# Kernel tuning notes

Hardware: AMD Instinct MI355X
Metric: run time of the kernel (lower is better)

Reference implementation:

```python
import jax, jax.numpy as jnp
from jax import lax
import numpy as np

# Config matching init_kwargs
NUM_CLASSES = 19
K = 200               # keep_k_centers
NMS_KERNEL = 9
CENTER_THR = 0.1
LABEL_DIV = 256
VOID = 255
STUFF_AREA = 4096
THING_IDS = np.array([11, 12, 13, 14, 15, 16, 17, 18])
IS_THING = jnp.zeros(NUM_CLASSES, bool).at[jnp.asarray(THING_IDS)].set(True)


def _process_one(logits, heat, offset):
    # logits [C,H,W], heat [1,H,W], offset [2,H,W]
    C, H, W = logits.shape
    sem = jnp.argmax(logits, axis=0).astype(jnp.int32)          # [H,W]
    h = heat[0]
    ht = jnp.where(h > CENTER_THR, h, 0.0)
    pad = NMS_KERNEL // 2
    # torch max_pool2d pads implicitly with -inf
    pooled = lax.reduce_window(ht, -jnp.inf, lax.max,
                               (NMS_KERNEL, NMS_KERNEL), (1, 1),
                               ((pad, pad), (pad, pad)))
    nms = jnp.where(ht == pooled, ht, 0.0)                      # [H,W]
    flat = nms.reshape(-1)
    scores, idx = lax.top_k(flat, K)                            # fixed-size center set
    valid = scores > 0.0
    num_pos = jnp.sum(flat > 0.0)
    # Match torch ordering: if more than K peaks -> topk (descending-score) order;
    # otherwise nonzero() row-major order. Invalid slots pushed to the end.
    big = jnp.int32(H * W + K)
    order_key = jnp.where(valid,
                          jnp.where(num_pos > K,
                                    jnp.arange(K, dtype=jnp.int32),
                                    idx.astype(jnp.int32)),
                          big)
    perm = jnp.argsort(order_key)
    idx = idx[perm]
    valid = valid[perm]
    FAR = 1e9  # invalid centers placed infinitely far away
    cy = jnp.where(valid, (idx // W).astype(jnp.float32), FAR)
    cx = jnp.where(valid, (idx % W).astype(jnp.float32), FAR)
    ty = jnp.arange(H, dtype=jnp.float32)[:, None] + offset[0]  # [H,W]
    tx = jnp.arange(W, dtype=jnp.float32)[None, :] + offset[1]  # [H,W]
    # squared distances [H,W,K]; argmin equals argmin of cdist
    d2 = (ty[..., None] - cy) ** 2 + (tx[..., None] - cx) ** 2
    closest = jnp.argmin(d2, axis=-1).astype(jnp.int32)         # [H,W]
    thing_mask = IS_THING[sem]
    inst = jnp.where(thing_mask & valid.any(), closest + 1, 0).astype(jnp.int32)
    # Majority class per instance via (instance, class) histogram.
    # argmax picks the smallest class among ties, matching torch.mode.
    hist = jnp.zeros((K + 1) * NUM_CLASSES, jnp.int32)
    hist = hist.at[(inst * NUM_CLASSES + sem).reshape(-1)].add(1)
    hist = hist.reshape(K + 1, NUM_CLASSES)
    majority = jnp.argmax(hist, axis=1).astype(jnp.int32)       # [K+1]
    pan = jnp.where(inst > 0, majority[inst] * LABEL_DIV + inst, VOID * LABEL_DIV)
    # Stuff: per-class pixel counts restricted to non-instance pixels
    stuff_pix = inst == 0
    skey = jnp.where(stuff_pix, sem, NUM_CLASSES).reshape(-1)
    scounts = jnp.zeros(NUM_CLASSES + 1, jnp.int32).at[skey].add(1)[:NUM_CLASSES]
    cond = stuff_pix & (~thing_mask) & (scounts[sem] >= STUFF_AREA)
    pan = jnp.where(cond, sem * LABEL_DIV, pan)
    return pan.astype(jnp.int32), inst


def setup_inputs() -> dict:
    key = jax.random.key(0)
    k1, k2, k3 = jax.random.split(key, 3)
    B, C, H, W = 2, NUM_CLASSES, 512, 1024
    semantic_logits = jax.random.normal(k1, (B, C, H, W), dtype=jnp.float32)
    center_heatmap = jax.random.uniform(k2, (B, 1, H, W), dtype=jnp.float32)
    offset_map = jax.random.normal(k3, (B, 2, H, W), dtype=jnp.float32)
    return {"semantic_logits": semantic_logits,
            "center_heatmap": center_heatmap,
            "offset_map": offset_map}


def reference(semantic_logits, center_heatmap, offset_map):
    pan, inst = jax.vmap(_process_one)(semantic_logits, center_heatmap, offset_map)
    return pan, inst
```

## Files before the change

### kernel.cpp

```cpp
#include <hip/hip_runtime.h>

#define B 2
#define C 19
#define H 512
#define W 1024
#define HW (H*W)
#define K 200
#define CAP 16384
#define SL 7680
#define NCLS 19
#define HISTN ((K+1)*NCLS)

typedef unsigned long long u64;


__global__ void k_zero(int* __restrict__ ws) {
    int i = blockIdx.x * 256 + threadIdx.x;
    if (i < 7680) ws[i] = 0;
}

__global__ __launch_bounds__(256) void k_nms(const float* __restrict__ heat,
                                             u64* __restrict__ keys,
                                             int* __restrict__ cnt) {
    __shared__ float ht[40][40];
    __shared__ float hm[40][32];
    __shared__ u64 lpk[1024];
    __shared__ int lcnt, gbase;
    int b = blockIdx.z;
    int x0 = blockIdx.x * 32, y0 = blockIdx.y * 32;
    int tid = threadIdx.y * 32 + threadIdx.x;
    const float* hb = heat + (size_t)b * HW;
    if (tid == 0) lcnt = 0;
    for (int i = tid; i < 40 * 40; i += 256) {
        int ly = i / 40, lx = i % 40;
        int gy = y0 + ly - 4, gx = x0 + lx - 4;
        float v = 0.f;
        if (gy >= 0 && gy < H && gx >= 0 && gx < W) {
            float hv = hb[gy * W + gx];
            v = (hv > 0.1f) ? hv : 0.f;
        }
        ht[ly][lx] = v;
    }
    __syncthreads();
    for (int i = tid; i < 40 * 32; i += 256) {
        int ly = i >> 5, lx = i & 31;
        float m = ht[ly][lx];
#pragma unroll
        for (int d = 1; d < 9; ++d) m = fmaxf(m, ht[ly][lx + d]);
        hm[ly][lx] = m;
    }
    __syncthreads();
#pragma unroll
    for (int r = 0; r < 4; ++r) {
        int oy = threadIdx.y + r * 8;
        int ox = threadIdx.x;
        float c = ht[oy + 4][ox + 4];
        if (c > 0.f) {
            float m = hm[oy][ox];
#pragma unroll
            for (int d = 1; d < 9; ++d) m = fmaxf(m, hm[oy + d][ox]);
            if (c == m) {
                int pos = atomicAdd(&lcnt, 1);
                unsigned sb = __float_as_uint(c);
                lpk[pos] = ((u64)(~sb) << 19)
                         | (unsigned)((y0 + oy) * W + (x0 + ox));
            }
        }
    }
    __syncthreads();
    if (tid == 0 && lcnt > 0) gbase = atomicAdd(&cnt[b], lcnt);
    __syncthreads();
    for (int i = tid; i < lcnt; i += 256) {
        int gp = gbase + i;
        if (gp < CAP) keys[(size_t)b * CAP + gp] = lpk[i];
    }
}

__global__ __launch_bounds__(1024) void k_topk(const u64* __restrict__ keys,
                                               const int* __restrict__ cnt,
                                               int* __restrict__ anyv,
                                               float* __restrict__ cy,
                                               float* __restrict__ cx) {
    __shared__ u64 skeys[SL];
    __shared__ int hcnt[256];
    __shared__ u64 cand[256];
    __shared__ u64 s_thr;
    __shared__ int sR, gcnt;
    int b = blockIdx.x, tid = threadIdx.x;
    int lane = tid & 63;
    const u64* kb = keys + (size_t)b * CAP;
    int N = cnt[b];
    int M = (N < CAP) ? N : CAP;
    int Ksel = (M < K) ? M : K;
    for (int i = tid; i < M && i < SL; i += 1024) skeys[i] = kb[i];
    if (tid == 0) { s_thr = 0ULL; sR = Ksel; gcnt = 0; }
    __syncthreads();
    u64 thr;
    if (M <= K) {
        thr = ~0ULL;
    } else {
#pragma unroll 1
        for (int d = 48; d >= 0; d -= 8) {
            if (tid < 256) hcnt[tid] = 0;
            __syncthreads();
            u64 pref = s_thr;
            for (int i = tid; i < M; i += 1024) {
                u64 kk = (i < SL) ? skeys[i] : kb[i];
                int dig = (int)((kk >> d) & 255ULL);
                if (d == 48) {
                    u64 mask = __ballot(1);
                    while (mask) {
                        int leader = __ffsll(mask) - 1;
                        int d0 = __shfl(dig, leader, 64);
                        u64 same = __ballot(dig == d0);
                        if (lane == leader) atomicAdd(&hcnt[d0], (int)__popcll(same));
                        mask &= ~same;
                    }
                } else {
                    if ((kk >> (d + 8)) == (pref >> (d + 8)))
                        atomicAdd(&hcnt[dig], 1);
                }
            }
            __syncthreads();
            if (tid < 64) {
                int h0 = hcnt[tid * 4 + 0], h1 = hcnt[tid * 4 + 1];
                int h2 = hcnt[tid * 4 + 2], h3 = hcnt[tid * 4 + 3];
                int s = h0 + h1 + h2 + h3;
                int incl = s;
#pragma unroll
                for (int off = 1; off < 64; off <<= 1) {
                    int v = __shfl_up(incl, off, 64);
                    if (tid >= off) incl += v;
                }
                int R = sR;
                int before = incl - s;
                if (before < R && R <= incl) {
                    int c = before, t = tid * 4;
                    if (c + h0 < R) { c += h0; t++;
                        if (c + h1 < R) { c += h1; t++;
                            if (c + h2 < R) { c += h2; t++; } } }
                    s_thr = pref | ((u64)t << d);
                    sR = R - c;
                }
            }
            __syncthreads();
        }
        thr = s_thr;
    }
    for (int i = tid; i < M; i += 1024) {
        u64 kk = (i < SL) ? skeys[i] : kb[i];
        if (kk <= thr) {
            int p = atomicAdd(&gcnt, 1);
            if (p < 256) cand[p] = kk;
        }
    }
    __syncthreads();
    if (tid < 256) {
        int g = (gcnt < 256) ? gcnt : 256;
        u64 v = (tid < g) ? cand[tid] : ~0ULL;
        if (N <= K && tid < g) v &= 0x7FFFFULL;
        cand[tid] = v;
    }
    __syncthreads();
    if (tid < 256) {
        u64 v = cand[tid];
        int r = 0;
        for (int j = 0; j < 256; ++j) {
            u64 cj = cand[j];
            r += (int)((cj < v) || (cj == v && j < tid));
        }
        skeys[r] = v;
    }
    __syncthreads();
    if (tid < K) {
        bool valid = tid < Ksel;
        unsigned idx = (unsigned)(skeys[tid] & 0x7FFFFULL);
        cy[b * K + tid] = valid ? (float)(idx >> 10) : 1e9f;
        cx[b * K + tid] = valid ? (float)(idx & 1023) : 1e9f;
    }
    if (tid == 0) anyv[b] = (N > 0) ? 1 : 0;
}

__global__ __launch_bounds__(256) void k_inst(const float* __restrict__ logits,
                                              const float* __restrict__ offs,
                                              const float* __restrict__ gcy,
                                              const float* __restrict__ gcx,
                                              const int* __restrict__ anyv,
                                              int* __restrict__ semout,
                                              int* __restrict__ inst,
                                              int* __restrict__ hist) {
    __shared__ int lh[HISTN];
    __shared__ float scy[K], scx[K];
    __shared__ unsigned char skk[K];
    __shared__ float red[4][8];
    __shared__ int wcnt[4];
    int b = blockIdx.z;
    int x0 = blockIdx.x << 5, y0 = blockIdx.y << 5;
    int tid = threadIdx.x;
    int lane = tid & 63, w = tid >> 6;
    for (int i = tid; i < HISTN; i += 256) lh[i] = 0;
    int r = tid >> 3;
    int c0 = (tid & 7) << 2;
    int gy = y0 + r;
    int gxb = x0 + c0;
    int q = (gy << 10) + gxb;
    const float* ob = offs + (size_t)b * 2 * HW;
    float4 oy4 = *(const float4*)(ob + q);
    float4 ox4 = *(const float4*)(ob + HW + q);
    int av = anyv[b];
    const float4* l4 = (const float4*)(logits + (size_t)b * C * HW) + (q >> 2);
    float4 v0 = l4[0];
    float best[4] = {v0.x, v0.y, v0.z, v0.w};
    int bc[4] = {0, 0, 0, 0};
#pragma unroll
    for (int c = 1; c < C; ++c) {
        float4 v = l4[(size_t)c * (HW / 4)];
        if (v.x > best[0]) { best[0] = v.x; bc[0] = c; }
        if (v.y > best[1]) { best[1] = v.y; bc[1] = c; }
        if (v.z > best[2]) { best[2] = v.z; bc[2] = c; }
        if (v.w > best[3]) { best[3] = v.w; bc[3] = c; }
    }
    float fy = (float)gy, fx = (float)gxb;
    float ty[4] = {fy + oy4.x, fy + oy4.y, fy + oy4.z, fy + oy4.w};
    float tx[4] = {fx + ox4.x, fx + 1.f + ox4.y, fx + 2.f + ox4.z, fx + 3.f + ox4.w};
    float tylo = fminf(fminf(ty[0], ty[1]), fminf(ty[2], ty[3]));
    float tyhi = fmaxf(fmaxf(ty[0], ty[1]), fmaxf(ty[2], ty[3]));
    float txlo = fminf(fminf(tx[0], tx[1]), fminf(tx[2], tx[3]));
    float txhi = fmaxf(fmaxf(tx[0], tx[1]), fmaxf(tx[2], tx[3]));
#pragma unroll
    for (int off = 32; off; off >>= 1) {
        tylo = fminf(tylo, __shfl_xor(tylo, off, 64));
        tyhi = fmaxf(tyhi, __shfl_xor(tyhi, off, 64));
        txlo = fminf(txlo, __shfl_xor(txlo, off, 64));
        txhi = fmaxf(txhi, __shfl_xor(txhi, off, 64));
    }
    if (lane == 0) { red[w][0] = tylo; red[w][1] = tyhi; red[w][2] = txlo; red[w][3] = txhi; }
    __syncthreads();
    tylo = fminf(fminf(red[0][0], red[1][0]), fminf(red[2][0], red[3][0]));
    tyhi = fmaxf(fmaxf(red[0][1], red[1][1]), fmaxf(red[2][1], red[3][1]));
    txlo = fminf(fminf(red[0][2], red[1][2]), fminf(red[2][2], red[3][2]));
    txhi = fmaxf(fmaxf(red[0][3], red[1][3]), fmaxf(red[2][3], red[3][3]));
    float kcy = 0.f, kcx = 0.f, mind2 = 0.f, maxd2 = 3.4e38f;
    if (tid < K) {
        kcy = gcy[b * K + tid]; kcx = gcx[b * K + tid];
        float dmy = fmaxf(fmaxf(tylo - kcy, kcy - tyhi), 0.f);
        float dMy = fmaxf(tyhi - kcy, kcy - tylo);
        float dmx = fmaxf(fmaxf(txlo - kcx, kcx - txhi), 0.f);
        float dMx = fmaxf(txhi - kcx, kcx - txlo);
        mind2 = dmy * dmy + dmx * dmx;
        maxd2 = dMy * dMy + dMx * dMx;
    }
    float mv = maxd2;
#pragma unroll
    for (int off = 32; off; off >>= 1) mv = fminf(mv, __shfl_xor(mv, off, 64));
    if (lane == 0) red[w][4] = mv;
    __syncthreads();
    float m = fminf(fminf(red[0][4], red[1][4]), fminf(red[2][4], red[3][4]));
    bool keep = (tid < K) && (mind2 <= m * 1.0001f + 1.0f);
    u64 bal = __ballot(keep);
    if (lane == 0) wcnt[w] = (int)__popcll(bal);
    __syncthreads();
    int nk = wcnt[0] + wcnt[1] + wcnt[2] + wcnt[3];
    if (keep) {
        int base = (w > 0 ? wcnt[0] : 0) + (w > 1 ? wcnt[1] : 0) + (w > 2 ? wcnt[2] : 0);
        int rank = base + (int)__popcll(bal & ((1ULL << lane) - 1ULL));
        scy[rank] = kcy; scx[rank] = kcx; skk[rank] = (unsigned char)tid;
    }
    __syncthreads();
    float bd[4] = {3.4e38f, 3.4e38f, 3.4e38f, 3.4e38f};
    int bi[4] = {0, 0, 0, 0};
    if (av) {
        for (int i = 0; i < nk; ++i) {
            float cyk = scy[i], cxk = scx[i];
#pragma unroll
            for (int j = 0; j < 4; ++j) {
                float dy = __fsub_rn(ty[j], cyk);
                float dx = __fsub_rn(tx[j], cxk);
                float d2 = __fadd_rn(__fmul_rn(dy, dy), __fmul_rn(dx, dx));
                if (d2 < bd[j]) { bd[j] = d2; bi[j] = i; }
            }
        }
    }
    int4 sem4, inst4;
    int* semp = (int*)&sem4;
    int* instp = (int*)&inst4;
#pragma unroll
    for (int j = 0; j < 4; ++j) {
        int s = bc[j];
        int ins = (s >= 11 && av) ? ((int)skk[bi[j]] + 1) : 0;
        semp[j] = s;
        instp[j] = ins;
        atomicAdd(&lh[ins * NCLS + s], 1);
    }
    *(int4*)(semout + b * HW + q) = sem4;
    *(int4*)(inst + b * HW + q) = inst4;
    __syncthreads();
    for (int i = tid; i < HISTN; i += 256)
        if (lh[i]) atomicAdd(&hist[b * HISTN + i], lh[i]);
}

__global__ void k_major(const int* __restrict__ hist, int* __restrict__ maj) {
    int r = blockIdx.x * 256 + threadIdx.x;
    if (r >= B * (K + 1)) return;
    int b = r / (K + 1), row = r % (K + 1);
    const int* h = hist + b * HISTN + row * NCLS;
    int best = h[0], bc = 0;
#pragma unroll
    for (int c2 = 1; c2 < NCLS; ++c2)
        if (h[c2] > best) { best = h[c2]; bc = c2; }
    maj[r] = bc;
}

__global__ __launch_bounds__(256) void k_pan(int* __restrict__ pansem,
                                             const int* __restrict__ inst,
                                             const int* __restrict__ hist,
                                             const int* __restrict__ maj) {
    int p = blockIdx.x * 256 + threadIdx.x;
    if (p >= B * HW) return;
    int b = p >> 19;
    int s = pansem[p];
    int in_ = inst[p];
    int pan;
    if (in_ > 0) {
        pan = maj[b * (K + 1) + in_] * 256 + in_;
    } else {
        pan = 255 * 256;
        if (s < 11 && hist[b * HISTN + s] >= 4096) pan = s * 256;
    }
    pansem[p] = pan;
}

extern "C" void kernel_launch(void* const* d_in, const int* in_sizes, int n_in,
                              void* d_out, int out_size, void* d_ws, size_t ws_size,
                              hipStream_t stream) {
    const float* logits = (const float*)d_in[0];
    const float* heat   = (const float*)d_in[1];
    const float* offs   = (const float*)d_in[2];
    int* out = (int*)d_out;
    int* pansem = out;
    int* inst = out + B * HW;
    int* wsi = (int*)d_ws;
    int* cnt  = wsi + 0;
    int* anyv = wsi + 4;
    int* hist = wsi + 16;
    int* maj  = wsi + 8192;
    float* cy = (float*)(wsi + 16384);
    float* cx = cy + B * K;
    u64* keys = (u64*)((char*)d_ws + 65536);

    k_zero<<<30, 256, 0, stream>>>(wsi);
    k_nms<<<dim3(W / 32, H / 32, B), dim3(32, 8, 1), 0, stream>>>(heat, keys, cnt);
    k_topk<<<B, 1024, 0, stream>>>(keys, cnt, anyv, cy, cx);
    k_inst<<<dim3(W / 32, H / 32, B), 256, 0, stream>>>(logits, offs, cy, cx, anyv, pansem, inst, hist);
    k_major<<<(B * (K + 1) + 255) / 256, 256, 0, stream>>>(hist, maj);
    k_pan<<<(B * HW + 255) / 256, 256, 0, stream>>>(pansem, inst, hist, maj);
}
```

Measured before the change: 79.87 us.

## Cut kernel launches, use per-block NMS slots, early-exit radix select, smaller inst tiles

Removes the zeroing kernel by having the top-k kernel clear the histogram, and makes NMS write each block's peaks into fixed slots with a per-block count instead of a global atomic append. Top-k prefix-sums the block counts and gathers the keys into shared memory. The radix select stops early once the threshold bin holds at most 256 keys. The majority-class pass is folded into the panoptic kernel, which now handles 8 pixels per thread with int4 accesses, and the instance kernel switches to 32x16 tiles with 128 threads. These changes cut launch overhead and raise parallelism in the pixel kernel, but they cap peaks at 128 per NMS block and 8192 in total, and they add serial gather work inside top-k.

```diff
diff --git a/kernel.cpp b/kernel.cpp
--- a/kernel.cpp
+++ b/kernel.cpp
@@ -6,28 +6,25 @@
 #define W 1024
 #define HW (H*W)
 #define K 200
-#define CAP 16384
-#define SL 7680
 #define NCLS 19
 #define HISTN ((K+1)*NCLS)
+#define NT 512
+#define MAXPB 128
+#define SL 8192
 
 typedef unsigned long long u64;
 
-
-__global__ void k_zero(int* __restrict__ ws) {
-    int i = blockIdx.x * 256 + threadIdx.x;
-    if (i < 7680) ws[i] = 0;
-}
 
 __global__ __launch_bounds__(256) void k_nms(const float* __restrict__ heat,
                                              u64* __restrict__ keys,
-                                             int* __restrict__ cnt) {
+                                             int* __restrict__ pcnt) {
     __shared__ float ht[40][40];
     __shared__ float hm[40][32];
     __shared__ u64 lpk[1024];
-    __shared__ int lcnt, gbase;
+    __shared__ int lcnt;
     int b = blockIdx.z;
     int x0 = blockIdx.x * 32, y0 = blockIdx.y * 32;
+    int gb = b * NT + blockIdx.y * 32 + blockIdx.x;
     int tid = threadIdx.y * 32 + threadIdx.x;
     const float* hb = heat + (size_t)b * HW;
     if (tid == 0) lcnt = 0;
@@ -68,16 +65,15 @@
         }
     }
     __syncthreads();
-    if (tid == 0 && lcnt > 0) gbase = atomicAdd(&cnt[b], lcnt);
-    __syncthreads();
-    for (int i = tid; i < lcnt; i += 256) {
-        int gp = gbase + i;
-        if (gp < CAP) keys[(size_t)b * CAP + gp] = lpk[i];
-    }
+    int n = (lcnt < MAXPB) ? lcnt : MAXPB;
+    if (tid == 0) pcnt[gb] = n;
+    for (int i = tid; i < n; i += 256)
+        keys[(size_t)gb * MAXPB + i] = lpk[i];
 }
 
 __global__ __launch_bounds__(1024) void k_topk(const u64* __restrict__ keys,
-                                               const int* __restrict__ cnt,
+                                               const int* __restrict__ pcnt,
+                                               int* __restrict__ hist,
                                                int* __restrict__ anyv,
                                                float* __restrict__ cy,
                                                float* __restrict__ cx) {
@@ -85,27 +81,49 @@
     __shared__ int hcnt[256];
     __shared__ u64 cand[256];
     __shared__ u64 s_thr;
-    __shared__ int sR, gcnt;
+    __shared__ int sR, gcnt, s_binc;
+    __shared__ int wsum[8];
     int b = blockIdx.x, tid = threadIdx.x;
-    int lane = tid & 63;
-    const u64* kb = keys + (size_t)b * CAP;
-    int N = cnt[b];
-    int M = (N < CAP) ? N : CAP;
+    int lane = tid & 63, w = tid >> 6;
+    for (int i = tid; i < HISTN; i += 1024) hist[b * HISTN + i] = 0;
+    int n = (tid < NT) ? pcnt[b * NT + tid] : 0;
+    int incl = n;
+#pragma unroll
+    for (int off = 1; off < 64; off <<= 1) {
+        int v = __shfl_up(incl, off, 64);
+        if (lane >= off) incl += v;
+    }
+    if (tid < NT && lane == 63) wsum[w] = incl;
+    __syncthreads();
+    int N = 0;
+#pragma unroll
+    for (int j = 0; j < 8; ++j) N += wsum[j];
+    int M = (N < SL) ? N : SL;
+    if (tid < NT && n > 0) {
+        int wbase = 0;
+        for (int j = 0; j < w; ++j) wbase += wsum[j];
+        int base = wbase + incl - n;
+        const u64* src = keys + (size_t)(b * NT + tid) * MAXPB;
+        for (int i = 0; i < n; ++i) {
+            int d = base + i;
+            if (d < SL) skeys[d] = src[i];
+        }
+    }
+    if (tid == 0) { s_thr = 0ULL; sR = (M < K) ? M : K; gcnt = 0; }
     int Ksel = (M < K) ? M : K;
-    for (int i = tid; i < M && i < SL; i += 1024) skeys[i] = kb[i];
-    if (tid == 0) { s_thr = 0ULL; sR = Ksel; gcnt = 0; }
     __syncthreads();
     u64 thr;
     if (M <= K) {
         thr = ~0ULL;
     } else {
+        bool done = false;
 #pragma unroll 1
-        for (int d = 48; d >= 0; d -= 8) {
+        for (int d = 48; d >= 0 && !done; d -= 8) {
             if (tid < 256) hcnt[tid] = 0;
             __syncthreads();
             u64 pref = s_thr;
             for (int i = tid; i < M; i += 1024) {
-                u64 kk = (i < SL) ? skeys[i] : kb[i];
+                u64 kk = skeys[i];
                 int dig = (int)((kk >> d) & 255ULL);
                 if (d == 48) {
                     u64 mask = __ballot(1);
@@ -126,29 +144,52 @@
                 int h0 = hcnt[tid * 4 + 0], h1 = hcnt[tid * 4 + 1];
                 int h2 = hcnt[tid * 4 + 2], h3 = hcnt[tid * 4 + 3];
                 int s = h0 + h1 + h2 + h3;
-                int incl = s;
+                int ic = s;
 #pragma unroll
                 for (int off = 1; off < 64; off <<= 1) {
-                    int v = __shfl_up(incl, off, 64);
-                    if (tid >= off) incl += v;
+                    int v = __shfl_up(ic, off, 64);
+                    if (tid >= off) ic += v;
                 }
                 int R = sR;
-                int before = incl - s;
-                if (before < R && R <= incl) {
+                int before = ic - s;
+                if (before < R && R <= ic) {
                     int c = before, t = tid * 4;
                     if (c + h0 < R) { c += h0; t++;
                         if (c + h1 < R) { c += h1; t++;
                             if (c + h2 < R) { c += h2; t++; } } }
                     s_thr = pref | ((u64)t << d);
                     sR = R - c;
+                    s_binc = hcnt[t];
                 }
             }
             __syncthreads();
+            if (s_binc <= 256) {
+                u64 p2 = s_thr;
+                for (int i = tid; i < M; i += 1024) {
+                    u64 kk = skeys[i];
+                    if ((kk >> d) == (p2 >> d)) {
+                        int p = atomicAdd(&gcnt, 1);
+                        if (p < 256) cand[p] = kk;
+                    }
+                }
+                __syncthreads();
+                int g = (gcnt < 256) ? gcnt : 256;
+                if (tid < g) {
+                    u64 v = cand[tid];
+                    int r = 0;
+                    for (int j = 0; j < g; ++j) r += (int)(cand[j] < v);
+                    if (r == sR - 1) s_thr = v;
+                }
+                __syncthreads();
+                if (tid == 0) gcnt = 0;
+                done = true;
+                __syncthreads();
+            }
         }
         thr = s_thr;
     }
     for (int i = tid; i < M; i += 1024) {
-        u64 kk = (i < SL) ? skeys[i] : kb[i];
+        u64 kk = skeys[i];
         if (kk <= thr) {
             int p = atomicAdd(&gcnt, 1);
             if (p < 256) cand[p] = kk;
@@ -181,7 +222,7 @@
     if (tid == 0) anyv[b] = (N > 0) ? 1 : 0;
 }
 
-__global__ __launch_bounds__(256) void k_inst(const float* __restrict__ logits,
+__global__ __launch_bounds__(128) void k_inst(const float* __restrict__ logits,
                                               const float* __restrict__ offs,
                                               const float* __restrict__ gcy,
                                               const float* __restrict__ gcx,
@@ -192,13 +233,13 @@
     __shared__ int lh[HISTN];
     __shared__ float scy[K], scx[K];
     __shared__ unsigned char skk[K];
-    __shared__ float red[4][8];
+    __shared__ float red[2][8];
     __shared__ int wcnt[4];
     int b = blockIdx.z;
-    int x0 = blockIdx.x << 5, y0 = blockIdx.y << 5;
+    int x0 = blockIdx.x << 5, y0 = blockIdx.y << 4;
     int tid = threadIdx.x;
     int lane = tid & 63, w = tid >> 6;
-    for (int i = tid; i < HISTN; i += 256) lh[i] = 0;
+    for (int i = tid; i < HISTN; i += 128) lh[i] = 0;
     int r = tid >> 3;
     int c0 = (tid & 7) << 2;
     int gy = y0 + r;
@@ -236,35 +277,50 @@
     }
     if (lane == 0) { red[w][0] = tylo; red[w][1] = tyhi; red[w][2] = txlo; red[w][3] = txhi; }
     __syncthreads();
-    tylo = fminf(fminf(red[0][0], red[1][0]), fminf(red[2][0], red[3][0]));
-    tyhi = fmaxf(fmaxf(red[0][1], red[1][1]), fmaxf(red[2][1], red[3][1]));
-    txlo = fminf(fminf(red[0][2], red[1][2]), fminf(red[2][2], red[3][2]));
-    txhi = fmaxf(fmaxf(red[0][3], red[1][3]), fmaxf(red[2][3], red[3][3]));
-    float kcy = 0.f, kcx = 0.f, mind2 = 0.f, maxd2 = 3.4e38f;
-    if (tid < K) {
-        kcy = gcy[b * K + tid]; kcx = gcx[b * K + tid];
-        float dmy = fmaxf(fmaxf(tylo - kcy, kcy - tyhi), 0.f);
-        float dMy = fmaxf(tyhi - kcy, kcy - tylo);
-        float dmx = fmaxf(fmaxf(txlo - kcx, kcx - txhi), 0.f);
-        float dMx = fmaxf(txhi - kcx, kcx - txlo);
-        mind2 = dmy * dmy + dmx * dmx;
-        maxd2 = dMy * dMy + dMx * dMx;
-    }
-    float mv = maxd2;
+    tylo = fminf(red[0][0], red[1][0]);
+    tyhi = fmaxf(red[0][1], red[1][1]);
+    txlo = fminf(red[0][2], red[1][2]);
+    txhi = fmaxf(red[0][3], red[1][3]);
+    float kcy0 = gcy[b * K + tid], kcx0 = gcx[b * K + tid];
+    float dmy = fmaxf(fmaxf(tylo - kcy0, kcy0 - tyhi), 0.f);
+    float dMy = fmaxf(tyhi - kcy0, kcy0 - tylo);
+    float dmx = fmaxf(fmaxf(txlo - kcx0, kcx0 - txhi), 0.f);
+    float dMx = fmaxf(txhi - kcx0, kcx0 - txlo);
+    float mind20 = dmy * dmy + dmx * dmx;
+    float maxd20 = dMy * dMy + dMx * dMx;
+    float kcy1 = 0.f, kcx1 = 0.f, mind21 = 0.f, maxd21 = 3.4e38f;
+    if (tid < K - 128) {
+        kcy1 = gcy[b * K + tid + 128]; kcx1 = gcx[b * K + tid + 128];
+        float ay = fmaxf(fmaxf(tylo - kcy1, kcy1 - tyhi), 0.f);
+        float My = fmaxf(tyhi - kcy1, kcy1 - tylo);
+        float ax = fmaxf(fmaxf(txlo - kcx1, kcx1 - txhi), 0.f);
+        float Mx = fmaxf(txhi - kcx1, kcx1 - txlo);
+        mind21 = ay * ay + ax * ax;
+        maxd21 = My * My + Mx * Mx;
+    }
+    float mv = fminf(maxd20, maxd21);
 #pragma unroll
     for (int off = 32; off; off >>= 1) mv = fminf(mv, __shfl_xor(mv, off, 64));
     if (lane == 0) red[w][4] = mv;
     __syncthreads();
-    float m = fminf(fminf(red[0][4], red[1][4]), fminf(red[2][4], red[3][4]));
-    bool keep = (tid < K) && (mind2 <= m * 1.0001f + 1.0f);
-    u64 bal = __ballot(keep);
-    if (lane == 0) wcnt[w] = (int)__popcll(bal);
-    __syncthreads();
-    int nk = wcnt[0] + wcnt[1] + wcnt[2] + wcnt[3];
-    if (keep) {
-        int base = (w > 0 ? wcnt[0] : 0) + (w > 1 ? wcnt[1] : 0) + (w > 2 ? wcnt[2] : 0);
-        int rank = base + (int)__popcll(bal & ((1ULL << lane) - 1ULL));
-        scy[rank] = kcy; scx[rank] = kcx; skk[rank] = (unsigned char)tid;
+    float m = fminf(red[0][4], red[1][4]);
+    float cut = m * 1.0001f + 1.0f;
+    bool keep0 = mind20 <= cut;
+    bool keep1 = (tid < K - 128) && (mind21 <= cut);
+    u64 bal0 = __ballot(keep0);
+    u64 bal1 = __ballot(keep1);
+    if (lane == 0) { wcnt[w] = (int)__popcll(bal0); wcnt[2 + w] = (int)__popcll(bal1); }
+    __syncthreads();
+    int nk01 = wcnt[0] + wcnt[1];
+    int nk = nk01 + wcnt[2] + wcnt[3];
+    u64 low = (1ULL << lane) - 1ULL;
+    if (keep0) {
+        int rank = (w ? wcnt[0] : 0) + (int)__popcll(bal0 & low);
+        scy[rank] = kcy0; scx[rank] = kcx0; skk[rank] = (unsigned char)tid;
+    }
+    if (keep1) {
+        int rank = nk01 + (w ? wcnt[2] : 0) + (int)__popcll(bal1 & low);
+        scy[rank] = kcy1; scx[rank] = kcx1; skk[rank] = (unsigned char)(tid + 128);
     }
     __syncthreads();
     float bd[4] = {3.4e38f, 3.4e38f, 3.4e38f, 3.4e38f};
@@ -295,39 +351,54 @@
     *(int4*)(semout + b * HW + q) = sem4;
     *(int4*)(inst + b * HW + q) = inst4;
     __syncthreads();
-    for (int i = tid; i < HISTN; i += 256)
+    for (int i = tid; i < HISTN; i += 128)
         if (lh[i]) atomicAdd(&hist[b * HISTN + i], lh[i]);
 }
 
-__global__ void k_major(const int* __restrict__ hist, int* __restrict__ maj) {
-    int r = blockIdx.x * 256 + threadIdx.x;
-    if (r >= B * (K + 1)) return;
-    int b = r / (K + 1), row = r % (K + 1);
-    const int* h = hist + b * HISTN + row * NCLS;
-    int best = h[0], bc = 0;
-#pragma unroll
-    for (int c2 = 1; c2 < NCLS; ++c2)
-        if (h[c2] > best) { best = h[c2]; bc = c2; }
-    maj[r] = bc;
-}
-
 __global__ __launch_bounds__(256) void k_pan(int* __restrict__ pansem,
                                              const int* __restrict__ inst,
-                                             const int* __restrict__ hist,
-                                             const int* __restrict__ maj) {
-    int p = blockIdx.x * 256 + threadIdx.x;
-    if (p >= B * HW) return;
-    int b = p >> 19;
-    int s = pansem[p];
-    int in_ = inst[p];
-    int pan;
-    if (in_ > 0) {
-        pan = maj[b * (K + 1) + in_] * 256 + in_;
-    } else {
-        pan = 255 * 256;
-        if (s < 11 && hist[b * HISTN + s] >= 4096) pan = s * 256;
-    }
-    pansem[p] = pan;
+                                             const int* __restrict__ hist) {
+    __shared__ int lh[HISTN];
+    __shared__ unsigned char maj[K + 1];
+    int b = blockIdx.x >> 8;
+    int blk = blockIdx.x & 255;
+    int tid = threadIdx.x;
+    const int* hb = hist + b * HISTN;
+    for (int i = tid; i < HISTN; i += 256) lh[i] = hb[i];
+    __syncthreads();
+    if (tid <= K) {
+        const int* h = &lh[tid * NCLS];
+        int best = h[0], bc = 0;
+#pragma unroll
+        for (int c = 1; c < NCLS; ++c)
+            if (h[c] > best) { best = h[c]; bc = c; }
+        maj[tid] = (unsigned char)bc;
+    }
+    __syncthreads();
+    int p0 = b * HW + blk * 2048;
+    const int4* s4 = (const int4*)(pansem + p0) + tid * 2;
+    const int4* i4 = (const int4*)(inst + p0) + tid * 2;
+    int4 sa = s4[0], sb = s4[1];
+    int4 ia = i4[0], ib = i4[1];
+    int4 pa, pb;
+    int* sp = (int*)&sa; int* ip = (int*)&ia; int* pp = (int*)&pa;
+#pragma unroll
+    for (int j = 0; j < 4; ++j) {
+        int s = sp[j], in_ = ip[j];
+        int pan = (in_ > 0) ? ((int)maj[in_] * 256 + in_)
+                 : ((s < 11 && lh[s] >= 4096) ? s * 256 : 65280);
+        pp[j] = pan;
+    }
+    sp = (int*)&sb; ip = (int*)&ib; pp = (int*)&pb;
+#pragma unroll
+    for (int j = 0; j < 4; ++j) {
+        int s = sp[j], in_ = ip[j];
+        int pan = (in_ > 0) ? ((int)maj[in_] * 256 + in_)
+                 : ((s < 11 && lh[s] >= 4096) ? s * 256 : 65280);
+        pp[j] = pan;
+    }
+    ((int4*)(pansem + p0))[tid * 2] = pa;
+    ((int4*)(pansem + p0))[tid * 2 + 1] = pb;
 }
 
 extern "C" void kernel_launch(void* const* d_in, const int* in_sizes, int n_in,
@@ -340,18 +411,15 @@
     int* pansem = out;
     int* inst = out + B * HW;
     int* wsi = (int*)d_ws;
-    int* cnt  = wsi + 0;
-    int* anyv = wsi + 4;
-    int* hist = wsi + 16;
-    int* maj  = wsi + 8192;
-    float* cy = (float*)(wsi + 16384);
+    int* hist = wsi;
+    float* cy = (float*)(wsi + 8192);
     float* cx = cy + B * K;
+    int* pcnt = wsi + 9216;
+    int* anyv = wsi + 10496;
     u64* keys = (u64*)((char*)d_ws + 65536);
 
-    k_zero<<<30, 256, 0, stream>>>(wsi);
-    k_nms<<<dim3(W / 32, H / 32, B), dim3(32, 8, 1), 0, stream>>>(heat, keys, cnt);
-    k_topk<<<B, 1024, 0, stream>>>(keys, cnt, anyv, cy, cx);
-    k_inst<<<dim3(W / 32, H / 32, B), 256, 0, stream>>>(logits, offs, cy, cx, anyv, pansem, inst, hist);
-    k_major<<<(B * (K + 1) + 255) / 256, 256, 0, stream>>>(hist, maj);
-    k_pan<<<(B * HW + 255) / 256, 256, 0, stream>>>(pansem, inst, hist, maj);
+    k_nms<<<dim3(32, 16, B), dim3(32, 8, 1), 0, stream>>>(heat, keys, pcnt);
+    k_topk<<<B, 1024, 0, stream>>>(keys, pcnt, hist, anyv, cy, cx);
+    k_inst<<<dim3(32, 32, B), 128, 0, stream>>>(logits, offs, cy, cx, anyv, pansem, inst, hist);
+    k_pan<<<B * 256, 256, 0, stream>>>(pansem, inst, hist);
 }
```

New measurement: 79.60 us. Within noise of the previous version (-0.3%).
